# Kernel tuning notes

Measured on AMD Instinct MI355X. Metric: run time of the kernel, lower is better.

Reference implementation:

```python
import jax, jax.numpy as jnp
import numpy as np

B, L, D, V = 256, 128, 1024, 32000
NEG_INF = -999.0  # matches the original -999 mask fill


def avgpool3_same(x):
    """tf.layers.average_pooling1d(pool=3, stride=1, padding='SAME').
    TF avg-pool excludes padded positions from the divisor, so edge
    positions average over 2 elements, interior over 3. x: [B, L, D]."""
    p = jnp.pad(x, ((0, 0), (1, 1), (0, 0)))
    summed = p[:, :-2] + p[:, 1:-1] + p[:, 2:]
    n = x.shape[1]
    counts = jnp.full((n,), 3.0, dtype=x.dtype).at[0].set(2.0).at[-1].set(2.0)
    return summed / counts[None, :, None]


def setup_inputs() -> dict:
    key = jax.random.key(0)
    k1, k2, k3, k4, k5, k6 = jax.random.split(key, 6)
    source_sent = jax.random.randint(k1, (B, L), 0, V, dtype=jnp.int32)
    target_sent = jax.random.randint(k2, (B, L), 0, V, dtype=jnp.int32)
    source_mask = jax.random.randint(k3, (B, L), 0, 2).astype(bool)
    target_mask = jax.random.randint(k4, (B, L), 0, 2).astype(bool)
    source_emb = jax.random.normal(k5, (V, D), dtype=jnp.float32) * 0.02
    target_emb = jax.random.normal(k6, (V, D), dtype=jnp.float32) * 0.02
    return {"source_sent": source_sent, "target_sent": target_sent,
            "source_mask": source_mask, "target_mask": target_mask,
            "source_emb": source_emb, "target_emb": target_emb}


def reference(source_sent, target_sent, source_mask, target_mask,
              source_emb, target_emb):
    # embedding lookup + avg-pool smoothing
    s = avgpool3_same(source_emb[source_sent])   # [B, S, D]
    t = avgpool3_same(target_emb[target_sent])   # [B, T, D]

    # mask: [B, S, T] = source valid AND target valid
    mask = source_mask[:, :, None] & target_mask[:, None, :]

    # target->source scores: [B, T, S]
    ta_score = jnp.einsum('btd,bsd->bts', t, s)
    ta_score = jnp.where(jnp.transpose(mask, (0, 2, 1)), ta_score, NEG_INF)
    ta_soft = jax.nn.softmax(ta_score, axis=-1)
    source_att = jnp.matmul(ta_soft, s)          # [B, T, D]

    # source->target scores reuse the transposed score matrix: [B, S, T]
    at_score = jnp.transpose(ta_score, (0, 2, 1))
    at_score = jnp.where(mask, at_score, NEG_INF)
    at_soft = jax.nn.softmax(at_score, axis=-1)
    target_att = jnp.matmul(at_soft, t)          # [B, S, D]

    return (s, source_att, at_soft, t, target_att, ta_soft)
```

## Files before the change

kernel.cpp:

```cpp
#include <hip/hip_runtime.h>
#include <hip/hip_bf16.h>
#include <stdint.h>


#define SL 128
#define DIM 1024

#define OFF_S     ((size_t)0)
#define OFF_SATT  ((size_t)33554432)
#define OFF_ATSM  ((size_t)67108864)
#define OFF_T     ((size_t)71303168)
#define OFF_TATT  ((size_t)104857600)
#define OFF_TASM  ((size_t)138412032)
#define SIDE_ELEMS ((size_t)33554432)
#define PHALF      ((size_t)4194304)
#define WS_NEEDED   ((size_t)134217728)
#define WS_P_NEEDED ((size_t)150994944)

typedef short bf16x8 __attribute__((ext_vector_type(8)));
typedef float f32x4 __attribute__((ext_vector_type(4)));
typedef unsigned short u16;

#define CH2   72
#define SC_LD 136
#define VT_LD 138

__device__ __forceinline__ u16 f2bf(float f) {
  union { float f; uint32_t u; } v; v.f = f;
  uint32_t r = (v.u + 0x7FFFu + ((v.u >> 16) & 1u)) >> 16;
  return (u16)r;
}
__device__ __forceinline__ float bf2f(u16 h) {
  union { uint32_t u; float f; } v; v.u = ((uint32_t)h) << 16;
  return v.f;
}

__global__ __launch_bounds__(256) void pool_kernel(
    const int* __restrict__ ssent, const int* __restrict__ tsent,
    const float* __restrict__ semb, const float* __restrict__ temb,
    float* __restrict__ out, u16* __restrict__ ws16, int use_ws)
{
  const int raw = blockIdx.x;
  const int bid = (raw & 7) * 512 + (raw >> 3);
  const int side = bid >> 11;
  const int rem = bid & 2047;
  const int b = rem >> 3;
  const int l0 = (rem & 7) * 16;
  const int tid = threadIdx.x;

  const int* __restrict__ sent = side ? tsent : ssent;
  const float* __restrict__ emb = side ? temb : semb;
  float* __restrict__ dst0 = out + (side ? OFF_T : OFF_S) + ((size_t)b * SL + l0) * DIM;
  u16* __restrict__ d16_0 = ws16 + (side ? SIDE_ELEMS : 0) + ((size_t)b * SL + l0) * DIM;

  const int sbase = b * SL + l0;
  float4 ePrev, eCur, eNext;
  if (l0 > 0) ePrev = ((const float4*)(emb + (size_t)sent[sbase - 1] * DIM))[tid];
  else        ePrev = (float4){0.f, 0.f, 0.f, 0.f};
  eCur = ((const float4*)(emb + (size_t)sent[sbase] * DIM))[tid];

  #pragma unroll
  for (int i = 0; i < 16; ++i) {
    const int l = l0 + i;
    if (l + 1 < SL)
      eNext = ((const float4*)(emb + (size_t)sent[sbase + i + 1] * DIM))[tid];
    else
      eNext = (float4){0.f, 0.f, 0.f, 0.f};
    const float scl = (l == 0 || l == SL - 1) ? 0.5f : (1.0f / 3.0f);
    f32x4 o;
    o[0] = (ePrev.x + eCur.x + eNext.x) * scl;
    o[1] = (ePrev.y + eCur.y + eNext.y) * scl;
    o[2] = (ePrev.z + eCur.z + eNext.z) * scl;
    o[3] = (ePrev.w + eCur.w + eNext.w) * scl;
    __builtin_nontemporal_store(o, ((f32x4*)(dst0 + (size_t)i * DIM)) + tid);
    if (use_ws) {
      ushort4 h;
      h.x = f2bf(o[0]); h.y = f2bf(o[1]); h.z = f2bf(o[2]); h.w = f2bf(o[3]);
      ((ushort4*)(d16_0 + (size_t)i * DIM))[tid] = h;
    }
    ePrev = eCur; eCur = eNext;
  }
}

__global__ __launch_bounds__(512) void score_kernel(
    const int* __restrict__ smask, const int* __restrict__ tmask,
    float* __restrict__ out, u16* __restrict__ ws16, int use_ws, int use_p16)
{
  __shared__ __align__(16) u16 chunkpool[2 * SL * CH2];
  __shared__ float part[2][4][SL];
  __shared__ float rowmax[SL], rowinv[SL], colmax[SL], colinv[SL];
  __shared__ float maskT[SL], maskS[SL];

  u16* const a_chunk = chunkpool;
  u16* const b_chunk = chunkpool + SL * CH2;
  u16* const score   = chunkpool;

  const int b = blockIdx.x;
  const int tid = threadIdx.x;
  const int lane = tid & 63;
  const int w = tid >> 6;

  const float* t_base = out + OFF_T + (size_t)b * SL * DIM;
  const float* s_base = out + OFF_S + (size_t)b * SL * DIM;
  float* ta_base = out + OFF_TASM + (size_t)b * SL * SL;
  float* at_base = out + OFF_ATSM + (size_t)b * SL * SL;
  u16* taP = ws16 + 2 * SIDE_ELEMS + (size_t)b * SL * SL;
  u16* atP = ws16 + 2 * SIDE_ELEMS + PHALF + (size_t)b * SL * SL;

  if (tid < SL) maskT[tid] = (tmask[b * SL + tid] != 0) ? 1.0f : 0.0f;
  else if (tid < 2 * SL) maskS[tid - SL] = (smask[b * SL + (tid - SL)] != 0) ? 1.0f : 0.0f;

  f32x4 acc[8];
  #pragma unroll
  for (int nt = 0; nt < 8; ++nt) acc[nt] = (f32x4){0.f, 0.f, 0.f, 0.f};

  const int srow = tid >> 2;
  const int seg = tid & 3;
  const size_t a_src = SIDE_ELEMS + ((size_t)b * SL + srow) * DIM + seg * 8;
  const size_t b_src = ((size_t)b * SL + srow) * DIM + seg * 8;
  u16* const a_dst = &a_chunk[srow * CH2 + seg * 8];
  u16* const b_dst = &b_chunk[srow * CH2 + seg * 8];

  uint4 ra0, ra1, rb0, rb1;

  if (use_ws) {
    ra0 = *(const uint4*)(ws16 + a_src);
    ra1 = *(const uint4*)(ws16 + a_src + 32);
    rb0 = *(const uint4*)(ws16 + b_src);
    rb1 = *(const uint4*)(ws16 + b_src + 32);
  }

  for (int it = 0; it < 16; ++it) {
    const int dk = it * 64;
    if (use_ws) {
      *(uint4*)a_dst = ra0;
      *(uint4*)(a_dst + 32) = ra1;
      *(uint4*)b_dst = rb0;
      *(uint4*)(b_dst + 32) = rb1;
    } else {
      #pragma unroll
      for (int c = 0; c < 2; ++c) {
        const float* ap = t_base + (size_t)srow * DIM + dk + c * 32 + seg * 8;
        const float* bp = s_base + (size_t)srow * DIM + dk + c * 32 + seg * 8;
        float4 va0 = ((const float4*)ap)[0], va1 = ((const float4*)ap)[1];
        float4 vb0 = ((const float4*)bp)[0], vb1 = ((const float4*)bp)[1];
        bf16x8 ha, hb;
        ha[0]=(short)f2bf(va0.x); ha[1]=(short)f2bf(va0.y); ha[2]=(short)f2bf(va0.z); ha[3]=(short)f2bf(va0.w);
        ha[4]=(short)f2bf(va1.x); ha[5]=(short)f2bf(va1.y); ha[6]=(short)f2bf(va1.z); ha[7]=(short)f2bf(va1.w);
        hb[0]=(short)f2bf(vb0.x); hb[1]=(short)f2bf(vb0.y); hb[2]=(short)f2bf(vb0.z); hb[3]=(short)f2bf(vb0.w);
        hb[4]=(short)f2bf(vb1.x); hb[5]=(short)f2bf(vb1.y); hb[6]=(short)f2bf(vb1.z); hb[7]=(short)f2bf(vb1.w);
        *(bf16x8*)(a_dst + c * 32) = ha;
        *(bf16x8*)(b_dst + c * 32) = hb;
      }
    }
    __syncthreads();

    if (use_ws && it + 1 < 16) {
      const int dk2 = dk + 64;
      ra0 = *(const uint4*)(ws16 + a_src + dk2);
      ra1 = *(const uint4*)(ws16 + a_src + dk2 + 32);
      rb0 = *(const uint4*)(ws16 + b_src + dk2);
      rb1 = *(const uint4*)(ws16 + b_src + dk2 + 32);
    }

    #pragma unroll
    for (int ks = 0; ks < 2; ++ks) {
      const int colb = ks * 32 + (lane >> 4) * 8;
      const bf16x8 afr = *(const bf16x8*)&a_chunk[(w * 16 + (lane & 15)) * CH2 + colb];
      #pragma unroll
      for (int nt = 0; nt < 8; ++nt) {
        const bf16x8 bfr = *(const bf16x8*)&b_chunk[(nt * 16 + (lane & 15)) * CH2 + colb];
        acc[nt] = __builtin_amdgcn_mfma_f32_16x16x32_bf16(afr, bfr, acc[nt], 0, 0, 0);
      }
    }
    __syncthreads();
  }

  #pragma unroll
  for (int nt = 0; nt < 8; ++nt) {
    const int coln = nt * 16 + (lane & 15);
    const float cm = maskS[coln];
    #pragma unroll
    for (int j = 0; j < 4; ++j) {
      const int rowm = w * 16 + (lane >> 4) * 4 + j;
      const float val = (cm != 0.0f && maskT[rowm] != 0.0f) ? acc[nt][j] : -999.0f;
      score[rowm * SC_LD + coln] = f2bf(val);
    }
  }
  __syncthreads();

  const int rc = tid & 127;
  const int q = tid >> 7;
  {
    float mx = -1e30f;
    #pragma unroll
    for (int c8 = 0; c8 < 4; ++c8) {
      const uint4 v = *(const uint4*)&score[rc * SC_LD + q * 32 + c8 * 8];
      mx = fmaxf(mx, fmaxf(bf2f((u16)(v.x & 0xffff)), bf2f((u16)(v.x >> 16))));
      mx = fmaxf(mx, fmaxf(bf2f((u16)(v.y & 0xffff)), bf2f((u16)(v.y >> 16))));
      mx = fmaxf(mx, fmaxf(bf2f((u16)(v.z & 0xffff)), bf2f((u16)(v.z >> 16))));
      mx = fmaxf(mx, fmaxf(bf2f((u16)(v.w & 0xffff)), bf2f((u16)(v.w >> 16))));
    }
    part[0][q][rc] = mx;
    float mc = -1e30f;
    #pragma unroll 8
    for (int r = q * 32; r < q * 32 + 32; ++r)
      mc = fmaxf(mc, bf2f(score[r * SC_LD + rc]));
    part[1][q][rc] = mc;
  }
  __syncthreads();
  if (tid < SL) {
    rowmax[tid] = fmaxf(fmaxf(part[0][0][tid], part[0][1][tid]),
                        fmaxf(part[0][2][tid], part[0][3][tid]));
  } else if (tid < 2 * SL) {
    const int c = tid - SL;
    colmax[c] = fmaxf(fmaxf(part[1][0][c], part[1][1][c]),
                      fmaxf(part[1][2][c], part[1][3][c]));
  }
  __syncthreads();
  {
    const float mR = rowmax[rc];
    float sm = 0.0f;
    #pragma unroll
    for (int c8 = 0; c8 < 4; ++c8) {
      const uint4 v = *(const uint4*)&score[rc * SC_LD + q * 32 + c8 * 8];
      sm += __expf(bf2f((u16)(v.x & 0xffff)) - mR) + __expf(bf2f((u16)(v.x >> 16)) - mR);
      sm += __expf(bf2f((u16)(v.y & 0xffff)) - mR) + __expf(bf2f((u16)(v.y >> 16)) - mR);
      sm += __expf(bf2f((u16)(v.z & 0xffff)) - mR) + __expf(bf2f((u16)(v.z >> 16)) - mR);
      sm += __expf(bf2f((u16)(v.w & 0xffff)) - mR) + __expf(bf2f((u16)(v.w >> 16)) - mR);
    }
    part[0][q][rc] = sm;
    const float mC = colmax[rc];
    float sc = 0.0f;
    #pragma unroll 8
    for (int r = q * 32; r < q * 32 + 32; ++r)
      sc += __expf(bf2f(score[r * SC_LD + rc]) - mC);
    part[1][q][rc] = sc;
  }
  __syncthreads();
  if (tid < SL) {
    rowinv[tid] = 1.0f / (part[0][0][tid] + part[0][1][tid] + part[0][2][tid] + part[0][3][tid]);
  } else if (tid < 2 * SL) {
    const int c = tid - SL;
    colinv[c] = 1.0f / (part[1][0][c] + part[1][1][c] + part[1][2][c] + part[1][3][c]);
  }
  __syncthreads();

  for (int idx = tid; idx < SL * SL; idx += 512) {
    const int r = idx >> 7, c = idx & 127;
    const float tv = __expf(bf2f(score[r * SC_LD + c]) - rowmax[r]) * rowinv[r];
    const float av = __expf(bf2f(score[c * SC_LD + r]) - colmax[r]) * colinv[r];
    __builtin_nontemporal_store(tv, &ta_base[idx]);
    __builtin_nontemporal_store(av, &at_base[idx]);
    if (use_p16) {
      taP[idx] = f2bf(tv);
      atP[idx] = f2bf(av);
    }
  }
}

__global__ __launch_bounds__(256) void pv_kernel(
    float* __restrict__ out, u16* __restrict__ ws16, int use_ws, int use_p16)
{
  __shared__ __align__(16) u16 vt[SL * VT_LD];

  const int raw = blockIdx.x;
  const int bid = (raw & 7) * 512 + (raw >> 3);
  const int ntile = bid & 7;
  const int b = (bid >> 3) & 255;
  const int ori = bid >> 11;
  const int tid = threadIdx.x;
  const int lane = tid & 63;
  const int w = tid >> 6;

  const float* p_base = out + (ori ? OFF_ATSM : OFF_TASM) + (size_t)b * SL * SL;
  const u16* p16_base = ws16 + 2 * SIDE_ELEMS + (ori ? PHALF : (size_t)0) + (size_t)b * SL * SL;
  float* att_base = out + (ori ? OFF_TATT : OFF_SATT) + (size_t)b * SL * DIM + ntile * 128;

  #pragma unroll
  for (int j = 0; j < 8; ++j) {
    const int idx = tid + j * 256;
    const int k = (idx & 15) | ((idx >> 8) << 4);
    const int oct = (idx >> 4) & 15;
    if (use_ws) {
      const u16* src = ws16 + (ori ? SIDE_ELEMS : 0)
                     + ((size_t)b * SL + k) * DIM + ntile * 128 + oct * 8;
      uint4 v = *(const uint4*)src;
      const u16* ev = (const u16*)&v;
      #pragma unroll
      for (int i = 0; i < 8; ++i) vt[(oct * 8 + i) * VT_LD + k] = ev[i];
    } else {
      const float* src = out + (ori ? OFF_T : OFF_S)
                       + ((size_t)b * SL + k) * DIM + ntile * 128 + oct * 8;
      float4 v0 = ((const float4*)src)[0];
      float4 v1 = ((const float4*)src)[1];
      vt[(oct * 8 + 0) * VT_LD + k] = f2bf(v0.x);
      vt[(oct * 8 + 1) * VT_LD + k] = f2bf(v0.y);
      vt[(oct * 8 + 2) * VT_LD + k] = f2bf(v0.z);
      vt[(oct * 8 + 3) * VT_LD + k] = f2bf(v0.w);
      vt[(oct * 8 + 4) * VT_LD + k] = f2bf(v1.x);
      vt[(oct * 8 + 5) * VT_LD + k] = f2bf(v1.y);
      vt[(oct * 8 + 6) * VT_LD + k] = f2bf(v1.z);
      vt[(oct * 8 + 7) * VT_LD + k] = f2bf(v1.w);
    }
  }

  bf16x8 afr[2][4];
  #pragma unroll
  for (int mt = 0; mt < 2; ++mt) {
    const int m = w * 32 + mt * 16 + (lane & 15);
    #pragma unroll
    for (int ks = 0; ks < 4; ++ks) {
      const int k0 = ks * 32 + (lane >> 4) * 8;
      if (use_p16) {
        afr[mt][ks] = *(const bf16x8*)(p16_base + (size_t)m * SL + k0);
      } else {
        const float* pp = p_base + (size_t)m * SL + k0;
        float4 x0 = ((const float4*)pp)[0];
        float4 x1 = ((const float4*)pp)[1];
        bf16x8 a;
        a[0] = (short)f2bf(x0.x); a[1] = (short)f2bf(x0.y);
        a[2] = (short)f2bf(x0.z); a[3] = (short)f2bf(x0.w);
        a[4] = (short)f2bf(x1.x); a[5] = (short)f2bf(x1.y);
        a[6] = (short)f2bf(x1.z); a[7] = (short)f2bf(x1.w);
        afr[mt][ks] = a;
      }
    }
  }
  __syncthreads();

  f32x4 acc[2][8];
  #pragma unroll
  for (int mt = 0; mt < 2; ++mt)
    #pragma unroll
    for (int nt = 0; nt < 8; ++nt)
      acc[mt][nt] = (f32x4){0.f, 0.f, 0.f, 0.f};

  const int colb = (lane >> 4) * 8;
  #pragma unroll
  for (int ks = 0; ks < 4; ++ks) {
    #pragma unroll
    for (int nt = 0; nt < 8; ++nt) {
      const bf16x8 bfr = *(const bf16x8*)&vt[(nt * 16 + (lane & 15)) * VT_LD + ks * 32 + colb];
      acc[0][nt] = __builtin_amdgcn_mfma_f32_16x16x32_bf16(afr[0][ks], bfr, acc[0][nt], 0, 0, 0);
      acc[1][nt] = __builtin_amdgcn_mfma_f32_16x16x32_bf16(afr[1][ks], bfr, acc[1][nt], 0, 0, 0);
    }
  }

  #pragma unroll
  for (int mt = 0; mt < 2; ++mt)
    #pragma unroll
    for (int nt = 0; nt < 8; ++nt) {
      const int rowm = w * 32 + mt * 16 + (lane >> 4) * 4;
      #pragma unroll
      for (int j = 0; j < 4; ++j)
        __builtin_nontemporal_store(acc[mt][nt][j],
            &att_base[(size_t)(rowm + j) * DIM + nt * 16 + (lane & 15)]);
    }
}

extern "C" void kernel_launch(void* const* d_in, const int* in_sizes, int n_in,
                              void* d_out, int out_size, void* d_ws, size_t ws_size,
                              hipStream_t stream) {
  const int* ssent = (const int*)d_in[0];
  const int* tsent = (const int*)d_in[1];
  const int* smask = (const int*)d_in[2];
  const int* tmask = (const int*)d_in[3];
  const float* semb = (const float*)d_in[4];
  const float* temb = (const float*)d_in[5];
  float* out = (float*)d_out;
  u16* ws16 = (u16*)d_ws;
  const int use_ws = (ws_size >= WS_NEEDED) ? 1 : 0;
  const int use_p16 = (ws_size >= WS_P_NEEDED) ? 1 : 0;

  hipLaunchKernelGGL(pool_kernel, dim3(4096), dim3(256), 0, stream,
                     ssent, tsent, semb, temb, out, ws16, use_ws);
  hipLaunchKernelGGL(score_kernel, dim3(256), dim3(512), 0, stream,
                     smask, tmask, out, ws16, use_ws, use_p16);
  hipLaunchKernelGGL(pv_kernel, dim3(4096), dim3(256), 0, stream, out, ws16, use_ws, use_p16);
}
```

Baseline: 246.0 us.

## Split score kernel per direction, recomputing scores to double block count

```diff
diff --git a/kernel.cpp b/kernel.cpp
--- a/kernel.cpp
+++ b/kernel.cpp
@@ -82,66 +82,75 @@
   }
 }
 
-__global__ __launch_bounds__(512) void score_kernel(
+__global__ __launch_bounds__(256) void score_kernel(
     const int* __restrict__ smask, const int* __restrict__ tmask,
     float* __restrict__ out, u16* __restrict__ ws16, int use_ws, int use_p16)
 {
   __shared__ __align__(16) u16 chunkpool[2 * SL * CH2];
-  __shared__ float part[2][4][SL];
-  __shared__ float rowmax[SL], rowinv[SL], colmax[SL], colinv[SL];
-  __shared__ float maskT[SL], maskS[SL];
+  __shared__ float part[2][SL];
+  __shared__ float rowmax[SL], rowinv[SL];
+  __shared__ float maskR[SL], maskC[SL];
 
   u16* const a_chunk = chunkpool;
   u16* const b_chunk = chunkpool + SL * CH2;
   u16* const score   = chunkpool;
 
-  const int b = blockIdx.x;
+  const int bid = blockIdx.x;
+  const int ori = bid >> 8;
+  const int b = bid & 255;
   const int tid = threadIdx.x;
   const int lane = tid & 63;
   const int w = tid >> 6;
 
-  const float* t_base = out + OFF_T + (size_t)b * SL * DIM;
-  const float* s_base = out + OFF_S + (size_t)b * SL * DIM;
-  float* ta_base = out + OFF_TASM + (size_t)b * SL * SL;
-  float* at_base = out + OFF_ATSM + (size_t)b * SL * SL;
-  u16* taP = ws16 + 2 * SIDE_ELEMS + (size_t)b * SL * SL;
-  u16* atP = ws16 + 2 * SIDE_ELEMS + PHALF + (size_t)b * SL * SL;
-
-  if (tid < SL) maskT[tid] = (tmask[b * SL + tid] != 0) ? 1.0f : 0.0f;
-  else if (tid < 2 * SL) maskS[tid - SL] = (smask[b * SL + (tid - SL)] != 0) ? 1.0f : 0.0f;
-
-  f32x4 acc[8];
-  #pragma unroll
-  for (int nt = 0; nt < 8; ++nt) acc[nt] = (f32x4){0.f, 0.f, 0.f, 0.f};
-
-  const int srow = tid >> 2;
-  const int seg = tid & 3;
-  const size_t a_src = SIDE_ELEMS + ((size_t)b * SL + srow) * DIM + seg * 8;
-  const size_t b_src = ((size_t)b * SL + srow) * DIM + seg * 8;
-  u16* const a_dst = &a_chunk[srow * CH2 + seg * 8];
-  u16* const b_dst = &b_chunk[srow * CH2 + seg * 8];
+  const size_t qoff = ori ? (size_t)0 : SIDE_ELEMS;
+  const size_t koff = ori ? SIDE_ELEMS : (size_t)0;
+  const float* qa_base = out + (ori ? OFF_S : OFF_T) + (size_t)b * SL * DIM;
+  const float* kb_base = out + (ori ? OFF_T : OFF_S) + (size_t)b * SL * DIM;
+  float* soft_base = out + (ori ? OFF_ATSM : OFF_TASM) + (size_t)b * SL * SL;
+  u16* pbase = ws16 + 2 * SIDE_ELEMS + (ori ? PHALF : (size_t)0) + (size_t)b * SL * SL;
+  const int* rmask = ori ? smask : tmask;
+  const int* cmask = ori ? tmask : smask;
+
+  if (tid < SL) maskR[tid] = (rmask[b * SL + tid] != 0) ? 1.0f : 0.0f;
+  else maskC[tid - SL] = (cmask[b * SL + (tid - SL)] != 0) ? 1.0f : 0.0f;
+
+  f32x4 acc[2][8];
+  #pragma unroll
+  for (int mt = 0; mt < 2; ++mt)
+    #pragma unroll
+    for (int nt = 0; nt < 8; ++nt)
+      acc[mt][nt] = (f32x4){0.f, 0.f, 0.f, 0.f};
+
+  const int srow = tid >> 1;
+  const int sg = tid & 1;
+  const size_t a_src = qoff + ((size_t)b * SL + srow) * DIM + sg * 16;
+  const size_t b_src = koff + ((size_t)b * SL + srow) * DIM + sg * 16;
+  u16* const a_dst = &a_chunk[srow * CH2 + sg * 16];
+  u16* const b_dst = &b_chunk[srow * CH2 + sg * 16];
 
   uint4 ra0, ra1, rb0, rb1;
+  uint4 ra2, ra3, rb2, rb3;
 
   if (use_ws) {
-    ra0 = *(const uint4*)(ws16 + a_src);
-    ra1 = *(const uint4*)(ws16 + a_src + 32);
-    rb0 = *(const uint4*)(ws16 + b_src);
-    rb1 = *(const uint4*)(ws16 + b_src + 32);
+    ra0 = *(const uint4*)(ws16 + a_src);       ra1 = *(const uint4*)(ws16 + a_src + 8);
+    ra2 = *(const uint4*)(ws16 + a_src + 32);  ra3 = *(const uint4*)(ws16 + a_src + 40);
+    rb0 = *(const uint4*)(ws16 + b_src);       rb1 = *(const uint4*)(ws16 + b_src + 8);
+    rb2 = *(const uint4*)(ws16 + b_src + 32);  rb3 = *(const uint4*)(ws16 + b_src + 40);
   }
 
   for (int it = 0; it < 16; ++it) {
     const int dk = it * 64;
     if (use_ws) {
-      *(uint4*)a_dst = ra0;
-      *(uint4*)(a_dst + 32) = ra1;
-      *(uint4*)b_dst = rb0;
-      *(uint4*)(b_dst + 32) = rb1;
+      *(uint4*)a_dst = ra0;        *(uint4*)(a_dst + 8) = ra1;
+      *(uint4*)(a_dst + 32) = ra2; *(uint4*)(a_dst + 40) = ra3;
+      *(uint4*)b_dst = rb0;        *(uint4*)(b_dst + 8) = rb1;
+      *(uint4*)(b_dst + 32) = rb2; *(uint4*)(b_dst + 40) = rb3;
     } else {
       #pragma unroll
-      for (int c = 0; c < 2; ++c) {
-        const float* ap = t_base + (size_t)srow * DIM + dk + c * 32 + seg * 8;
-        const float* bp = s_base + (size_t)srow * DIM + dk + c * 32 + seg * 8;
+      for (int c = 0; c < 4; ++c) {
+        const int co = (c < 2) ? (c * 8) : (16 + c * 8);
+        const float* ap = qa_base + (size_t)srow * DIM + dk + sg * 16 + co;
+        const float* bp = kb_base + (size_t)srow * DIM + dk + sg * 16 + co;
         float4 va0 = ((const float4*)ap)[0], va1 = ((const float4*)ap)[1];
         float4 vb0 = ((const float4*)bp)[0], vb1 = ((const float4*)bp)[1];
         bf16x8 ha, hb;
@@ -149,44 +158,49 @@
         ha[4]=(short)f2bf(va1.x); ha[5]=(short)f2bf(va1.y); ha[6]=(short)f2bf(va1.z); ha[7]=(short)f2bf(va1.w);
         hb[0]=(short)f2bf(vb0.x); hb[1]=(short)f2bf(vb0.y); hb[2]=(short)f2bf(vb0.z); hb[3]=(short)f2bf(vb0.w);
         hb[4]=(short)f2bf(vb1.x); hb[5]=(short)f2bf(vb1.y); hb[6]=(short)f2bf(vb1.z); hb[7]=(short)f2bf(vb1.w);
-        *(bf16x8*)(a_dst + c * 32) = ha;
-        *(bf16x8*)(b_dst + c * 32) = hb;
+        *(bf16x8*)(a_dst + co) = ha;
+        *(bf16x8*)(b_dst + co) = hb;
       }
     }
     __syncthreads();
 
     if (use_ws && it + 1 < 16) {
       const int dk2 = dk + 64;
-      ra0 = *(const uint4*)(ws16 + a_src + dk2);
-      ra1 = *(const uint4*)(ws16 + a_src + dk2 + 32);
-      rb0 = *(const uint4*)(ws16 + b_src + dk2);
-      rb1 = *(const uint4*)(ws16 + b_src + dk2 + 32);
+      ra0 = *(const uint4*)(ws16 + a_src + dk2);       ra1 = *(const uint4*)(ws16 + a_src + dk2 + 8);
+      ra2 = *(const uint4*)(ws16 + a_src + dk2 + 32);  ra3 = *(const uint4*)(ws16 + a_src + dk2 + 40);
+      rb0 = *(const uint4*)(ws16 + b_src + dk2);       rb1 = *(const uint4*)(ws16 + b_src + dk2 + 8);
+      rb2 = *(const uint4*)(ws16 + b_src + dk2 + 32);  rb3 = *(const uint4*)(ws16 + b_src + dk2 + 40);
     }
 
     #pragma unroll
     for (int ks = 0; ks < 2; ++ks) {
       const int colb = ks * 32 + (lane >> 4) * 8;
-      const bf16x8 afr = *(const bf16x8*)&a_chunk[(w * 16 + (lane & 15)) * CH2 + colb];
+      bf16x8 afr[2];
+      afr[0] = *(const bf16x8*)&a_chunk[(w * 32 + (lane & 15)) * CH2 + colb];
+      afr[1] = *(const bf16x8*)&a_chunk[(w * 32 + 16 + (lane & 15)) * CH2 + colb];
       #pragma unroll
       for (int nt = 0; nt < 8; ++nt) {
         const bf16x8 bfr = *(const bf16x8*)&b_chunk[(nt * 16 + (lane & 15)) * CH2 + colb];
-        acc[nt] = __builtin_amdgcn_mfma_f32_16x16x32_bf16(afr, bfr, acc[nt], 0, 0, 0);
+        acc[0][nt] = __builtin_amdgcn_mfma_f32_16x16x32_bf16(afr[0], bfr, acc[0][nt], 0, 0, 0);
+        acc[1][nt] = __builtin_amdgcn_mfma_f32_16x16x32_bf16(afr[1], bfr, acc[1][nt], 0, 0, 0);
       }
     }
     __syncthreads();
   }
 
   #pragma unroll
-  for (int nt = 0; nt < 8; ++nt) {
-    const int coln = nt * 16 + (lane & 15);
-    const float cm = maskS[coln];
-    #pragma unroll
-    for (int j = 0; j < 4; ++j) {
-      const int rowm = w * 16 + (lane >> 4) * 4 + j;
-      const float val = (cm != 0.0f && maskT[rowm] != 0.0f) ? acc[nt][j] : -999.0f;
-      score[rowm * SC_LD + coln] = f2bf(val);
-    }
-  }
+  for (int mt = 0; mt < 2; ++mt)
+    #pragma unroll
+    for (int nt = 0; nt < 8; ++nt) {
+      const int coln = nt * 16 + (lane & 15);
+      const float cm = maskC[coln];
+      #pragma unroll
+      for (int j = 0; j < 4; ++j) {
+        const int rowm = w * 32 + mt * 16 + (lane >> 4) * 4 + j;
+        const float val = (cm != 0.0f && maskR[rowm] != 0.0f) ? acc[mt][nt][j] : -999.0f;
+        score[rowm * SC_LD + coln] = f2bf(val);
+      }
+    }
   __syncthreads();
 
   const int rc = tid & 127;
@@ -194,68 +208,40 @@
   {
     float mx = -1e30f;
     #pragma unroll
-    for (int c8 = 0; c8 < 4; ++c8) {
-      const uint4 v = *(const uint4*)&score[rc * SC_LD + q * 32 + c8 * 8];
+    for (int c8 = 0; c8 < 8; ++c8) {
+      const uint4 v = *(const uint4*)&score[rc * SC_LD + q * 64 + c8 * 8];
       mx = fmaxf(mx, fmaxf(bf2f((u16)(v.x & 0xffff)), bf2f((u16)(v.x >> 16))));
       mx = fmaxf(mx, fmaxf(bf2f((u16)(v.y & 0xffff)), bf2f((u16)(v.y >> 16))));
       mx = fmaxf(mx, fmaxf(bf2f((u16)(v.z & 0xffff)), bf2f((u16)(v.z >> 16))));
       mx = fmaxf(mx, fmaxf(bf2f((u16)(v.w & 0xffff)), bf2f((u16)(v.w >> 16))));
     }
-    part[0][q][rc] = mx;
-    float mc = -1e30f;
-    #pragma unroll 8
-    for (int r = q * 32; r < q * 32 + 32; ++r)
-      mc = fmaxf(mc, bf2f(score[r * SC_LD + rc]));
-    part[1][q][rc] = mc;
-  }
-  __syncthreads();
-  if (tid < SL) {
-    rowmax[tid] = fmaxf(fmaxf(part[0][0][tid], part[0][1][tid]),
-                        fmaxf(part[0][2][tid], part[0][3][tid]));
-  } else if (tid < 2 * SL) {
-    const int c = tid - SL;
-    colmax[c] = fmaxf(fmaxf(part[1][0][c], part[1][1][c]),
-                      fmaxf(part[1][2][c], part[1][3][c]));
-  }
+    part[q][rc] = mx;
+  }
+  __syncthreads();
+  if (tid < SL) rowmax[tid] = fmaxf(part[0][tid], part[1][tid]);
   __syncthreads();
   {
     const float mR = rowmax[rc];
     float sm = 0.0f;
     #pragma unroll
-    for (int c8 = 0; c8 < 4; ++c8) {
-      const uint4 v = *(const uint4*)&score[rc * SC_LD + q * 32 + c8 * 8];
+    for (int c8 = 0; c8 < 8; ++c8) {
+      const uint4 v = *(const uint4*)&score[rc * SC_LD + q * 64 + c8 * 8];
       sm += __expf(bf2f((u16)(v.x & 0xffff)) - mR) + __expf(bf2f((u16)(v.x >> 16)) - mR);
       sm += __expf(bf2f((u16)(v.y & 0xffff)) - mR) + __expf(bf2f((u16)(v.y >> 16)) - mR);
       sm += __expf(bf2f((u16)(v.z & 0xffff)) - mR) + __expf(bf2f((u16)(v.z >> 16)) - mR);
       sm += __expf(bf2f((u16)(v.w & 0xffff)) - mR) + __expf(bf2f((u16)(v.w >> 16)) - mR);
     }
-    part[0][q][rc] = sm;
-    const float mC = colmax[rc];
-    float sc = 0.0f;
-    #pragma unroll 8
-    for (int r = q * 32; r < q * 32 + 32; ++r)
-      sc += __expf(bf2f(score[r * SC_LD + rc]) - mC);
-    part[1][q][rc] = sc;
-  }
-  __syncthreads();
-  if (tid < SL) {
-    rowinv[tid] = 1.0f / (part[0][0][tid] + part[0][1][tid] + part[0][2][tid] + part[0][3][tid]);
-  } else if (tid < 2 * SL) {
-    const int c = tid - SL;
-    colinv[c] = 1.0f / (part[1][0][c] + part[1][1][c] + part[1][2][c] + part[1][3][c]);
-  }
-  __syncthreads();
-
-  for (int idx = tid; idx < SL * SL; idx += 512) {
+    part[q][rc] = sm;
+  }
+  __syncthreads();
+  if (tid < SL) rowinv[tid] = 1.0f / (part[0][tid] + part[1][tid]);
+  __syncthreads();
+
+  for (int idx = tid; idx < SL * SL; idx += 256) {
     const int r = idx >> 7, c = idx & 127;
     const float tv = __expf(bf2f(score[r * SC_LD + c]) - rowmax[r]) * rowinv[r];
-    const float av = __expf(bf2f(score[c * SC_LD + r]) - colmax[r]) * colinv[r];
-    __builtin_nontemporal_store(tv, &ta_base[idx]);
-    __builtin_nontemporal_store(av, &at_base[idx]);
-    if (use_p16) {
-      taP[idx] = f2bf(tv);
-      atP[idx] = f2bf(av);
-    }
+    soft_base[idx] = tv;
+    if (use_p16) pbase[idx] = f2bf(tv);
   }
 }
 
@@ -354,8 +340,7 @@
       const int rowm = w * 32 + mt * 16 + (lane >> 4) * 4;
       #pragma unroll
       for (int j = 0; j < 4; ++j)
-        __builtin_nontemporal_store(acc[mt][nt][j],
-            &att_base[(size_t)(rowm + j) * DIM + nt * 16 + (lane & 15)]);
+        att_base[(size_t)(rowm + j) * DIM + nt * 16 + (lane & 15)] = acc[mt][nt][j];
     }
 }
 
@@ -375,7 +360,7 @@
 
   hipLaunchKernelGGL(pool_kernel, dim3(4096), dim3(256), 0, stream,
                      ssent, tsent, semb, temb, out, ws16, use_ws);
-  hipLaunchKernelGGL(score_kernel, dim3(256), dim3(512), 0, stream,
+  hipLaunchKernelGGL(score_kernel, dim3(512), dim3(256), 0, stream,
                      smask, tmask, out, ws16, use_ws, use_p16);
   hipLaunchKernelGGL(pv_kernel, dim3(4096), dim3(256), 0, stream, out, ws16, use_ws, use_p16);
 }
```

Result: slower. 282.4 us (+14.8%).
